# Performance work log

Measured on AMD Instinct MI355X. Metric: run time of the kernel, lower is better.

The kernel has to match this reference:

```python
import math
import jax, jax.numpy as jnp
import numpy as np

VMIN, VMAX, NUM_BINS = 0.0, 1.0, 64
BIN_WIDTH = (VMAX - VMIN) / NUM_BINS
SIGMA = BIN_WIDTH * (1.0 / (2.0 * math.sqrt(2.0 * math.log(2.0))))
EPS = 1e-10


def setup_inputs() -> dict:
    key = jax.random.key(0)
    kx, ky = jax.random.split(key)
    shape = (2, 1, 96, 96, 96)
    x = jax.random.uniform(kx, shape, dtype=jnp.float32)
    y = jax.random.uniform(ky, shape, dtype=jnp.float32)
    return {"x": x, "y": y}


def _gauss_win(v, bins):
    # v: (N, P), bins: (B,) -> (N, B, P)
    d = v[:, None, :] - bins[None, :, None]
    # NOTE: faithful to source: exp(.)/sqrt(2*pi) * sigma (multiplies by sigma)
    return jnp.exp(-(d * d) / (2.0 * SIGMA * SIGMA)) / math.sqrt(2.0 * math.pi) * SIGMA


def reference(x, y):
    N = x.shape[0]
    xf = x.reshape(N, -1)  # (N, P); dim=1 channel folded into P
    yf = y.reshape(N, -1)
    bins = jnp.linspace(VMIN, VMAX, NUM_BINS, dtype=x.dtype)
    win_x = _gauss_win(xf, bins)  # (N, B, P)
    win_y = _gauss_win(yf, bins)  # (N, B, P)
    hist_joint = jnp.einsum('nbp,ncp->nbc', win_x, win_y)  # (N, B, B)
    hist_norm = hist_joint.sum(axis=(1, 2)) + EPS
    p_joint = hist_joint / hist_norm[:, None, None]
    p_x = p_joint.sum(axis=2)
    p_y = p_joint.sum(axis=1)
    ent_x = -jnp.sum(p_x * jnp.log(p_x + EPS), axis=1)
    ent_y = -jnp.sum(p_y * jnp.log(p_y + EPS), axis=1)
    ent_joint = -jnp.sum(p_joint * jnp.log(p_joint + EPS), axis=(1, 2))
    # normalised=True branch
    return -jnp.mean((ent_x + ent_y) / ent_joint)
```

## Files before the change

### kernel.cpp

```cpp
#include <hip/hip_runtime.h>
#include <math.h>


#define NBINS 64
#define LDA2 72
#define TILEH (NBINS * LDA2)

typedef _Float16 half8    __attribute__((ext_vector_type(8)));
typedef float    floatx16 __attribute__((ext_vector_type(16)));

static constexpr double kSigmaD = 0.015625 / 2.3548200450309493;
static constexpr double kAcD    = (1.0 / (63.0 * 63.0)) / (2.0 * kSigmaD * kSigmaD);
static constexpr float  kAc     = (float)kAcD;
static constexpr float  kEps    = 1e-10f;

__global__ void zero_ws_kernel(float* __restrict__ hist, float* __restrict__ out, int n) {
    int i = blockIdx.x * blockDim.x + threadIdx.x;
    if (i < n) hist[i] = 0.0f;
    if (i == 0) out[0] = 0.0f;
}

__global__ __launch_bounds__(128, 2) void hist_gemm_kernel(
        const float* __restrict__ x, const float* __restrict__ y,
        float* __restrict__ hist, int P, int elemsPerWave) {
    __shared__ __align__(16) _Float16 tiles[2][2][NBINS][LDA2];

    const int t    = threadIdx.x;
    const int lane = t & 63;
    const int wave = t >> 6;
    const int n    = blockIdx.y;

    _Float16* __restrict__ Ax = &tiles[wave][0][0][0];
    _Float16* __restrict__ By = &tiles[wave][1][0][0];

    {
        float4* p4 = (float4*)Ax;
        const int n16 = 2 * TILEH * 2 / 16;
        for (int i = lane; i < n16; i += 64) p4[i] = float4{0.f, 0.f, 0.f, 0.f};
    }

    floatx16 acc[2][2] = {};
    const float* __restrict__ xp = x + (size_t)n * P;
    const float* __restrict__ yp = y + (size_t)n * P;

    const int waveBase = (blockIdx.x * 2 + wave) * elemsPerWave;
    int lim = P - waveBase;
    if (lim > elemsPerWave) lim = elemsPerWave;
    const int nChunks = (elemsPerWave + 63) / 64;

#define GLOAD(c2, ox, oy) do {                                   \
        int off_ = (c2) * 64 + lane;                             \
        int g_ = waveBase + ((off_ < lim) ? off_ : 0);           \
        g_ = min(g_, P - 1);                                     \
        ox = xp[g_]; oy = yp[g_];                                \
    } while (0)

    int pcx = 2, pcy = 2;
    float vx, vy;
    GLOAD(0, vx, vy);

    for (int c = 0; c < nChunks; ++c) {
        float nvx = 0.f, nvy = 0.f;
        if (c + 1 < nChunks) GLOAD(c + 1, nvx, nvy);

        const bool valid = (c * 64 + lane) < lim;
        float wx[5], wy[5];
        int cx = 2, cy = 2;
        if (valid) {
            const float sx = vx * 63.0f;
            const float sy = vy * 63.0f;
            cx = min(max((int)(sx + 0.5f), 2), 61);
            cy = min(max((int)(sy + 0.5f), 2), 61);
            const float dx = sx - (float)cx;
            const float dy = sy - (float)cy;
#pragma unroll
            for (int k = 0; k < 5; ++k) {
                const float ddx = dx - (float)(k - 2);
                const float ddy = dy - (float)(k - 2);
                wx[k] = __expf(-kAc * ddx * ddx);
                wy[k] = __expf(-kAc * ddy * ddy);
            }
        } else {
#pragma unroll
            for (int k = 0; k < 5; ++k) { wx[k] = 0.0f; wy[k] = 0.0f; }
        }

#pragma unroll
        for (int k = 0; k < 5; ++k) {
            Ax[(pcx - 2 + k) * LDA2 + lane] = (_Float16)0.0f;
            By[(pcy - 2 + k) * LDA2 + lane] = (_Float16)0.0f;
        }
#pragma unroll
        for (int k = 0; k < 5; ++k) {
            Ax[(cx - 2 + k) * LDA2 + lane] = (_Float16)wx[k];
            By[(cy - 2 + k) * LDA2 + lane] = (_Float16)wy[k];
        }
        pcx = cx; pcy = cy;

        const int mrow = lane & 31;
        const int kq   = 8 * (lane >> 5);
        const _Float16* pa = &Ax[mrow * LDA2 + kq];
        const _Float16* pb = &By[mrow * LDA2 + kq];
#pragma unroll
        for (int kb = 0; kb < 4; ++kb) {
            const half8 a0 = *(const half8*)(pa + kb * 16);
            const half8 a1 = *(const half8*)(pa + 32 * LDA2 + kb * 16);
            const half8 b0 = *(const half8*)(pb + kb * 16);
            const half8 b1 = *(const half8*)(pb + 32 * LDA2 + kb * 16);
            acc[0][0] = __builtin_amdgcn_mfma_f32_32x32x16_f16(a0, b0, acc[0][0], 0, 0, 0);
            acc[0][1] = __builtin_amdgcn_mfma_f32_32x32x16_f16(a0, b1, acc[0][1], 0, 0, 0);
            acc[1][0] = __builtin_amdgcn_mfma_f32_32x32x16_f16(a1, b0, acc[1][0], 0, 0, 0);
            acc[1][1] = __builtin_amdgcn_mfma_f32_32x32x16_f16(a1, b1, acc[1][1], 0, 0, 0);
        }

        vx = nvx; vy = nvy;
    }
#undef GLOAD

    float* wsum = (float*)&tiles[wave][0][0][0];
#pragma unroll
    for (int qi = 0; qi < 2; ++qi)
#pragma unroll
        for (int qj = 0; qj < 2; ++qj)
#pragma unroll
            for (int r = 0; r < 16; ++r) {
                const int row = qi * 32 + (r & 3) + 8 * (r >> 2) + 4 * (lane >> 5);
                const int col = qj * 32 + (lane & 31);
                wsum[row * NBINS + col] = acc[qi][qj][r];
            }
    __syncthreads();

    float* __restrict__ gh = hist + (size_t)n * NBINS * NBINS;
    const float* w0 = (const float*)&tiles[0][0][0][0];
    const float* w1 = (const float*)&tiles[1][0][0][0];
    for (int i = t; i < NBINS * NBINS; i += 128) {
        atomicAdd(&gh[i], w0[i] + w1[i]);
    }
}

__device__ __forceinline__ float block_sum_bcast(float v, float* sm) {
#pragma unroll
    for (int off = 32; off > 0; off >>= 1) v += __shfl_down(v, off, 64);
    __syncthreads();
    const int lane = threadIdx.x & 63;
    const int wid  = threadIdx.x >> 6;
    if (lane == 0) sm[wid] = v;
    __syncthreads();
    return sm[0] + sm[1] + sm[2] + sm[3];
}

__global__ __launch_bounds__(256) void finalize_kernel(
        const float* __restrict__ hist, float* __restrict__ out) {
    __shared__ float sm[4];
    __shared__ float sx[NBINS];
    __shared__ float sy[NBINS];

    const int n = blockIdx.x;
    const float* __restrict__ h = hist + (size_t)n * NBINS * NBINS;

    float s = 0.0f;
    for (int i = threadIdx.x; i < NBINS * NBINS; i += 256) s += h[i];
    const float S = block_sum_bcast(s, sm) + kEps;
    const float invS = 1.0f / S;

    float ej = 0.0f;
    for (int i = threadIdx.x; i < NBINS * NBINS; i += 256) {
        const float p = h[i] * invS;
        ej += p * __logf(p + kEps);
    }

    if (threadIdx.x < NBINS) {
        float px = 0.0f;
        const float* rp = &h[threadIdx.x * NBINS];
        for (int c = 0; c < NBINS; c++) px += rp[c];
        px *= invS;
        sx[threadIdx.x] = px * __logf(px + kEps);
    } else if (threadIdx.x < 2 * NBINS) {
        const int c = threadIdx.x - NBINS;
        float py = 0.0f;
        for (int b = 0; b < NBINS; b++) py += h[b * NBINS + c];
        py *= invS;
        sy[c] = py * __logf(py + kEps);
    }

    const float EJ = block_sum_bcast(ej, sm);
    const float mx = (threadIdx.x < NBINS) ? sx[threadIdx.x] : 0.0f;
    const float my = (threadIdx.x < NBINS) ? sy[threadIdx.x] : 0.0f;
    const float EX = block_sum_bcast(mx, sm);
    const float EY = block_sum_bcast(my, sm);

    if (threadIdx.x == 0) atomicAdd(out, -0.5f * ((EX + EY) / EJ));
}

extern "C" void kernel_launch(void* const* d_in, const int* in_sizes, int n_in,
                              void* d_out, int out_size, void* d_ws, size_t ws_size,
                              hipStream_t stream) {
    const float* x = (const float*)d_in[0];
    const float* y = (const float*)d_in[1];
    float* hist = (float*)d_ws;
    float* out  = (float*)d_out;

    const int N = 2;
    const int P = in_sizes[0] / N;
    const int blocksPerN   = 512;
    const int elemsPerWave = P / (blocksPerN * 2);

    const int histElems = N * NBINS * NBINS;
    zero_ws_kernel<<<(histElems + 255) / 256, 256, 0, stream>>>(hist, out, histElems);

    dim3 grid(blocksPerN, N);
    hist_gemm_kernel<<<grid, 128, 0, stream>>>(x, y, hist, P, elemsPerWave);

    finalize_kernel<<<2, 256, 0, stream>>>(hist, out);
}
```

Measured before the change: 103.6 us.

## Fuse finalize into histogram kernel via last-block completion counter

Drops the separate finalize kernel. The last block of the histogram kernel, detected with an atomic completion counter, now computes the entropies and writes the output directly. The zeroing kernel is replaced with hipMemsetAsync, which also clears the counter. The intent is to save launch overhead and the gaps between kernels, at the cost of one serial block running the reduction over both histograms at the end.

Result: slower. 155.8 us (+50.3%).

```diff
diff --git a/kernel.cpp b/kernel.cpp
--- a/kernel.cpp
+++ b/kernel.cpp
@@ -14,16 +14,22 @@
 static constexpr float  kAc     = (float)kAcD;
 static constexpr float  kEps    = 1e-10f;
 
-__global__ void zero_ws_kernel(float* __restrict__ hist, float* __restrict__ out, int n) {
-    int i = blockIdx.x * blockDim.x + threadIdx.x;
-    if (i < n) hist[i] = 0.0f;
-    if (i == 0) out[0] = 0.0f;
+__device__ __forceinline__ float bsum128(float v, volatile float* sm) {
+#pragma unroll
+    for (int off = 32; off > 0; off >>= 1) v += __shfl_down(v, off, 64);
+    __syncthreads();
+    if ((threadIdx.x & 63) == 0) sm[threadIdx.x >> 6] = v;
+    __syncthreads();
+    return sm[0] + sm[1];
 }
 
 __global__ __launch_bounds__(128, 2) void hist_gemm_kernel(
         const float* __restrict__ x, const float* __restrict__ y,
-        float* __restrict__ hist, int P, int elemsPerWave) {
+        float* __restrict__ hist, int* __restrict__ counter,
+        float* __restrict__ out, int P, int elemsPerWave, int totalBlocks) {
     __shared__ __align__(16) _Float16 tiles[2][2][NBINS][LDA2];
+    __shared__ float smr[2];
+    __shared__ int   sIsLast;
 
     const int t    = threadIdx.x;
     const int lane = t & 63;
@@ -136,60 +142,57 @@
     for (int i = t; i < NBINS * NBINS; i += 128) {
         atomicAdd(&gh[i], w0[i] + w1[i]);
     }
-}
-
-__device__ __forceinline__ float block_sum_bcast(float v, float* sm) {
-#pragma unroll
-    for (int off = 32; off > 0; off >>= 1) v += __shfl_down(v, off, 64);
-    __syncthreads();
-    const int lane = threadIdx.x & 63;
-    const int wid  = threadIdx.x >> 6;
-    if (lane == 0) sm[wid] = v;
-    __syncthreads();
-    return sm[0] + sm[1] + sm[2] + sm[3];
-}
-
-__global__ __launch_bounds__(256) void finalize_kernel(
-        const float* __restrict__ hist, float* __restrict__ out) {
-    __shared__ float sm[4];
-    __shared__ float sx[NBINS];
-    __shared__ float sy[NBINS];
-
-    const int n = blockIdx.x;
-    const float* __restrict__ h = hist + (size_t)n * NBINS * NBINS;
-
-    float s = 0.0f;
-    for (int i = threadIdx.x; i < NBINS * NBINS; i += 256) s += h[i];
-    const float S = block_sum_bcast(s, sm) + kEps;
-    const float invS = 1.0f / S;
-
-    float ej = 0.0f;
-    for (int i = threadIdx.x; i < NBINS * NBINS; i += 256) {
-        const float p = h[i] * invS;
-        ej += p * __logf(p + kEps);
-    }
-
-    if (threadIdx.x < NBINS) {
-        float px = 0.0f;
-        const float* rp = &h[threadIdx.x * NBINS];
-        for (int c = 0; c < NBINS; c++) px += rp[c];
-        px *= invS;
-        sx[threadIdx.x] = px * __logf(px + kEps);
-    } else if (threadIdx.x < 2 * NBINS) {
-        const int c = threadIdx.x - NBINS;
-        float py = 0.0f;
-        for (int b = 0; b < NBINS; b++) py += h[b * NBINS + c];
-        py *= invS;
-        sy[c] = py * __logf(py + kEps);
-    }
-
-    const float EJ = block_sum_bcast(ej, sm);
-    const float mx = (threadIdx.x < NBINS) ? sx[threadIdx.x] : 0.0f;
-    const float my = (threadIdx.x < NBINS) ? sy[threadIdx.x] : 0.0f;
-    const float EX = block_sum_bcast(mx, sm);
-    const float EY = block_sum_bcast(my, sm);
-
-    if (threadIdx.x == 0) atomicAdd(out, -0.5f * ((EX + EY) / EJ));
+
+    __threadfence();
+    __syncthreads();
+    if (t == 0) {
+        int done = __hip_atomic_fetch_add(counter, 1, __ATOMIC_ACQ_REL,
+                                          __HIP_MEMORY_SCOPE_AGENT);
+        sIsLast = (done == totalBlocks - 1);
+    }
+    __syncthreads();
+    if (!sIsLast) return;
+
+    float* hl = (float*)&tiles[0][0][0][0];
+    for (int i = t; i < 2 * NBINS * NBINS; i += 128)
+        hl[i] = __hip_atomic_load(&hist[i], __ATOMIC_RELAXED,
+                                  __HIP_MEMORY_SCOPE_AGENT);
+    __syncthreads();
+
+    float res = 0.0f;
+    for (int n2 = 0; n2 < 2; ++n2) {
+        const float* h = hl + n2 * NBINS * NBINS;
+
+        float s = 0.0f;
+        for (int i = t; i < NBINS * NBINS; i += 128) s += h[i];
+        const float S = bsum128(s, smr) + kEps;
+        const float invS = 1.0f / S;
+
+        float ej = 0.0f;
+        for (int i = t; i < NBINS * NBINS; i += 128) {
+            const float p = h[i] * invS;
+            ej += p * __logf(p + kEps);
+        }
+        const float EJ = bsum128(ej, smr);
+
+        float m = 0.0f;
+        if (t < NBINS) {
+            float px = 0.0f;
+            const float* rp = &h[t * NBINS];
+            for (int c2 = 0; c2 < NBINS; ++c2) px += rp[(c2 + t) & 63];
+            px *= invS;
+            m = px * __logf(px + kEps);
+        } else {
+            const int c2 = t - NBINS;
+            float py = 0.0f;
+            for (int b = 0; b < NBINS; ++b) py += h[b * NBINS + c2];
+            py *= invS;
+            m = py * __logf(py + kEps);
+        }
+        const float EXY = bsum128(m, smr);
+        res += EXY / EJ;
+    }
+    if (t == 0) out[0] = -0.5f * res;
 }
 
 extern "C" void kernel_launch(void* const* d_in, const int* in_sizes, int n_in,
@@ -197,19 +200,19 @@
                               hipStream_t stream) {
     const float* x = (const float*)d_in[0];
     const float* y = (const float*)d_in[1];
-    float* hist = (float*)d_ws;
-    float* out  = (float*)d_out;
+    float* hist    = (float*)d_ws;
+    int*   counter = (int*)((char*)d_ws + 2 * NBINS * NBINS * sizeof(float));
+    float* out     = (float*)d_out;
 
     const int N = 2;
     const int P = in_sizes[0] / N;
     const int blocksPerN   = 512;
     const int elemsPerWave = P / (blocksPerN * 2);
-
-    const int histElems = N * NBINS * NBINS;
-    zero_ws_kernel<<<(histElems + 255) / 256, 256, 0, stream>>>(hist, out, histElems);
+    const int totalBlocks  = blocksPerN * N;
+
+    hipMemsetAsync(d_ws, 0, 2 * NBINS * NBINS * sizeof(float) + 64, stream);
 
     dim3 grid(blocksPerN, N);
-    hist_gemm_kernel<<<grid, 128, 0, stream>>>(x, y, hist, P, elemsPerWave);
-
-    finalize_kernel<<<2, 256, 0, stream>>>(hist, out);
+    hist_gemm_kernel<<<grid, 128, 0, stream>>>(x, y, hist, counter, out,
+                                               P, elemsPerWave, totalBlocks);
 }
```
